# Optimization experiments

Hardware: AMD Instinct MI355X
Metric: run time of the kernel (lower is better)

## Reference

```python
import jax, jax.numpy as jnp
import numpy as np
from jax import lax

IN_CHANNELS = 4
STEPS_IN_ITR = 3


def one_step_ltm(x, T):
    # x: [B, H, W]; T: [B, 10, H, W] (9 stencil weight planes + bias plane)
    B, H, W = x.shape
    xp = jnp.pad(x, ((0, 0), (1, 1), (1, 1)))
    out = T[:, 9]
    k = 0
    # original ordering: X0..X2 scan row-offset with col-offset 0, X3..X5 col 1, X6..X8 col 2
    for dj in range(3):
        for di in range(3):
            out = out + xp[:, di:di + H, dj:dj + W] * T[:, k]
            k += 1
    return out


def setup_inputs() -> dict:
    key = jax.random.key(0)
    k1, k2, k3 = jax.random.split(key, 3)
    B, Tt, C, H, W = 8, 16, 1, 512, 512
    x = jax.random.uniform(k1, (B, Tt, C, H, W), dtype=jnp.float32)
    # stand-in unet: 3x3 SAME conv, in_channels -> 10
    W_unet = jax.random.normal(k2, (10, IN_CHANNELS, 3, 3), dtype=jnp.float32) * 0.1
    b_unet = jax.random.normal(k3, (10,), dtype=jnp.float32) * 0.1
    return {"x": x, "W_unet": W_unet, "b_unet": b_unet}


def reference(x, W_unet, b_unet):
    B, Tt, C, H, W = x.shape
    x_in = x[:, -IN_CHANNELS:, 0]  # [B, in_channels, H, W]
    T = lax.conv_general_dilated(
        x_in, W_unet, window_strides=(1, 1), padding='SAME',
        dimension_numbers=('NCHW', 'OIHW', 'NCHW')) + b_unet[None, :, None, None]

    xt0 = one_step_ltm(x[:, -1, 0], T)  # stored at t=0 WITHOUT sigmoid (as in original)

    def body(xt, _):
        for _j in range(STEPS_IN_ITR):
            xt = one_step_ltm(xt, T)
            xt = jax.nn.sigmoid(one_step_ltm(xt, T))
        return xt, xt

    _, xs = lax.scan(body, xt0, None, length=Tt - 1)  # [Tt-1, B, H, W]
    seq = jnp.concatenate([xt0[None], xs], axis=0)     # [Tt, B, H, W]
    seq = jnp.transpose(seq, (1, 0, 2, 3))             # [B, Tt, H, W]
    xout = jnp.zeros((B, Tt, C, H, W), dtype=x.dtype).at[:, :, 0].set(seq)
    return xout
```

## Files before the change

### kernel.cpp

```cpp
#include <hip/hip_runtime.h>
#include <hip/hip_fp16.h>
#include <math.h>

#define Bd 8
#define Td 16
#define Hd 512
#define Wd 512
#define HWc (Hd * Wd)
#define NPIX (Bd * HWc)

#define CTW 128
#define CTH 8
#define CRW 130
#define CRH 10
#define CPITCH 132
#define CTHR 512

#define TS   64
#define H6   6
#define RS   76
#define LP   77
#define NTHR 768
#define RPG  8
#define NG   10

__global__ __launch_bounds__(CTHR)
void conv_step0_kernel(const float* __restrict__ x,
                       const float* __restrict__ Wu,
                       const float* __restrict__ bu,
                       __half2* __restrict__ T,
                       float* __restrict__ out) {
    __shared__ __align__(16) float sX[4][CRH][CPITCH];

    int bx  = blockIdx.x;
    int b   = bx >> 8;
    int rem = bx & 255;
    int by  = rem >> 2;
    int bc  = rem & 3;
    int i0  = by * CTH;
    int j0  = bc * CTW;

    const float* xb = x + ((size_t)b * Td + 12) * HWc;
    int tid = threadIdx.x;

    for (int idx = tid; idx < 4 * CRH * CRW; idx += CTHR) {
        int ch = idx / (CRH * CRW);
        int r2 = idx - ch * (CRH * CRW);
        int r  = r2 / CRW;
        int c  = r2 - r * CRW;
        int gi = i0 + r - 1, gj = j0 + c - 1;
        float v = 0.0f;
        if ((unsigned)gi < (unsigned)Hd && (unsigned)gj < (unsigned)Wd)
            v = xb[(size_t)ch * HWc + gi * Wd + gj];
        sX[ch][r][c] = v;
    }
    __syncthreads();

    int tx = tid & 63;
    int ty = tid >> 6;

    float t0[10], t1[10];
    #pragma unroll
    for (int o = 0; o < 10; ++o) { float bv = bu[o]; t0[o] = bv; t1[o] = bv; }

    #pragma unroll
    for (int ch = 0; ch < 4; ++ch)
        #pragma unroll
        for (int kh = 0; kh < 3; ++kh) {
            const float* rp = &sX[ch][ty + kh][2 * tx];
            float2 a  = *(const float2*)rp;
            float2 b2 = *(const float2*)(rp + 2);
            float w0 = a.x, w1 = a.y, w2 = b2.x, w3 = b2.y;
            #pragma unroll
            for (int o = 0; o < 10; ++o) {
                float wt0 = Wu[((o * 4 + ch) * 3 + kh) * 3 + 0];
                float wt1 = Wu[((o * 4 + ch) * 3 + kh) * 3 + 1];
                float wt2 = Wu[((o * 4 + ch) * 3 + kh) * 3 + 2];
                t0[o] += w0 * wt0 + w1 * wt1 + w2 * wt2;
                t1[o] += w1 * wt0 + w2 * wt1 + w3 * wt2;
            }
        }

    int gi = i0 + ty;
    int gjv = j0 + 2 * tx;
    size_t pix = (size_t)gi * Wd + gjv;
    __half2* Tb = T + (size_t)b * 5 * HWc;
    #pragma unroll
    for (int q = 0; q < 5; ++q) {
        __half2 h0 = __floats2half2_rn(t0[2 * q], t0[2 * q + 1]);
        __half2 h1 = __floats2half2_rn(t1[2 * q], t1[2 * q + 1]);
        uint2 pk;
        pk.x = *(unsigned*)&h0;
        pk.y = *(unsigned*)&h1;
        *(uint2*)(Tb + (size_t)q * HWc + pix) = pk;
    }

    float o0 = t0[9], o1 = t1[9];
    #pragma unroll
    for (int di = 0; di < 3; ++di) {
        const float* rp = &sX[3][ty + di][2 * tx];
        float2 a  = *(const float2*)rp;
        float2 b2 = *(const float2*)(rp + 2);
        float w0 = a.x, w1 = a.y, w2 = b2.x, w3 = b2.y;
        #pragma unroll
        for (int dj = 0; dj < 3; ++dj) {
            float xa = (dj == 0) ? w0 : ((dj == 1) ? w1 : w2);
            float xc = (dj == 0) ? w1 : ((dj == 1) ? w2 : w3);
            o0 += xa * t0[dj * 3 + di];
            o1 += xc * t1[dj * 3 + di];
        }
    }
    float2 ov; ov.x = o0; ov.y = o1;
    *(float2*)(out + (size_t)b * Td * HWc + pix) = ov;
}

__global__ __launch_bounds__(NTHR, 6)
void fused6_vstrip_kernel(const float* __restrict__ xin,
                          const __half2* __restrict__ T,
                          float* __restrict__ xout) {
    __shared__ float sA[RS * LP];
    __shared__ float sB[RS * LP];

    int tile = blockIdx.x;
    int b   = tile >> 6;
    int trr = (tile >> 3) & 7;
    int tcc = tile & 7;
    int ri = trr * TS - H6;
    int rj = tcc * TS - H6;

    const float* xb = xin + (size_t)b * Td * HWc;
    const __half2* Tb = T + (size_t)b * 5 * HWc;
    int tid = threadIdx.x;

    for (int idx = tid; idx < RS * RS; idx += NTHR) {
        int r = idx / RS, c = idx - r * RS;
        int gi = ri + r, gj = rj + c;
        float v = 0.0f;
        if ((unsigned)gi < (unsigned)Hd && (unsigned)gj < (unsigned)Wd)
            v = xb[gi * Wd + gj];
        sA[r * LP + c] = v;
    }
    for (int idx = tid; idx < 4 * RS; idx += NTHR) {
        int side = idx / RS, k = idx - side * RS;
        int r, c;
        if (side == 0)      { r = 0;      c = k; }
        else if (side == 1) { r = RS - 1; c = k; }
        else if (side == 2) { r = k;      c = 0; }
        else                { r = k;      c = RS - 1; }
        sB[r * LP + c] = 0.0f;
    }

    int g  = tid / RS;
    int c  = tid - g * RS;
    int rs = 1 + g * RPG;
    bool colint = (c >= 1) && (c <= RS - 2);
    bool active = (g < NG) && colint;
    int  gj     = rj + c;
    bool colin  = (unsigned)gj < (unsigned)Wd;

    __half2 treg[RPG][5];
    #pragma unroll
    for (int jj = 0; jj < RPG; ++jj) {
        int r  = rs + jj;
        int gi = ri + r;
        bool ok = active && (r <= RS - 2) && ((unsigned)gi < (unsigned)Hd) && colin;
        #pragma unroll
        for (int q = 0; q < 5; ++q)
            treg[jj][q] = ok ? Tb[(size_t)q * HWc + gi * Wd + gj]
                             : __floats2half2_rn(0.0f, 0.0f);
    }
    __syncthreads();

    float* cur = sA;
    float* nxt = sB;

    #pragma unroll
    for (int s = 1; s <= 6; ++s) {
        if (active) {
            float w00 = cur[(rs - 1) * LP + c - 1];
            float w01 = cur[(rs - 1) * LP + c];
            float w02 = cur[(rs - 1) * LP + c + 1];
            float w10 = cur[rs * LP + c - 1];
            float w11 = cur[rs * LP + c];
            float w12 = cur[rs * LP + c + 1];
            #pragma unroll
            for (int jj = 0; jj < RPG; ++jj) {
                int r  = rs + jj;
                int r2 = (r + 1 <= RS - 1) ? (r + 1) : (RS - 1);
                float w20 = cur[r2 * LP + c - 1];
                float w21 = cur[r2 * LP + c];
                float w22 = cur[r2 * LP + c + 1];

                float2 p0 = __half22float2(treg[jj][0]);
                float2 p1 = __half22float2(treg[jj][1]);
                float2 p2 = __half22float2(treg[jj][2]);
                float2 p3 = __half22float2(treg[jj][3]);
                float2 p4 = __half22float2(treg[jj][4]);

                float a = p4.y
                        + w00 * p0.x + w10 * p0.y + w20 * p1.x
                        + w01 * p1.y + w11 * p2.x + w21 * p2.y
                        + w02 * p3.x + w12 * p3.y + w22 * p4.x;
                if ((s & 1) == 0) a = 1.0f / (1.0f + __expf(-a));

                int gi = ri + r;
                bool rowok = (r <= RS - 2);
                bool inimg = ((unsigned)gi < (unsigned)Hd) && colin;
                if (rowok) nxt[r * LP + c] = inimg ? a : 0.0f;

                w00 = w10; w01 = w11; w02 = w12;
                w10 = w20; w11 = w21; w12 = w22;
            }
        }
        __syncthreads();
        float* tmp = cur; cur = nxt; nxt = tmp;
    }

    float* ob = xout + (size_t)b * Td * HWc;
    for (int idx = tid; idx < TS * TS; idx += NTHR) {
        int rr = idx >> 6, cc = idx & 63;
        ob[(ri + H6 + rr) * Wd + (rj + H6 + cc)] = cur[(H6 + rr) * LP + (H6 + cc)];
    }
}

extern "C" void kernel_launch(void* const* d_in, const int* in_sizes, int n_in,
                              void* d_out, int out_size, void* d_ws, size_t ws_size,
                              hipStream_t stream) {
    const float* x  = (const float*)d_in[0];
    const float* Wu = (const float*)d_in[1];
    const float* bu = (const float*)d_in[2];
    float* out = (float*)d_out;
    __half2* T = (__half2*)d_ws;

    conv_step0_kernel<<<2048, CTHR, 0, stream>>>(x, Wu, bu, T, out);

    for (int t = 1; t < Td; ++t)
        fused6_vstrip_kernel<<<512, NTHR, 0, stream>>>(out + (size_t)(t - 1) * HWc, T,
                                                       out + (size_t)t * HWc);
}
```

Measured before the change: 572.6 us.

## Replace per-timestep launches with persistent cooperative kernel using grid sync

Replaces the 15 separate per-timestep stencil kernel launches with one cooperative persistent kernel of 256 blocks, each handling two tiles and looping over timesteps with grid.sync between them. The T coefficients for both tiles are loaded into registers once and kept across all timesteps, removing repeated T reads and launch gaps. In exchange, register pressure roughly doubles for treg, occupancy drops, and each grid-wide barrier adds synchronization cost. The two tiles per block are processed serially.

```diff
diff --git a/kernel.cpp b/kernel.cpp
--- a/kernel.cpp
+++ b/kernel.cpp
@@ -1,6 +1,9 @@
 #include <hip/hip_runtime.h>
 #include <hip/hip_fp16.h>
+#include <hip/hip_cooperative_groups.h>
 #include <math.h>
+
+namespace cg = cooperative_groups;
 
 #define Bd 8
 #define Td 16
@@ -112,6 +115,134 @@
     }
     float2 ov; ov.x = o0; ov.y = o1;
     *(float2*)(out + (size_t)b * Td * HWc + pix) = ov;
+}
+
+__global__ __launch_bounds__(NTHR, 4)
+void scan_persistent2_kernel(const __half2* __restrict__ T,
+                             float* __restrict__ out) {
+    cg::grid_group grid = cg::this_grid();
+
+    __shared__ float sA[RS * LP];
+    __shared__ float sB[RS * LP];
+
+    int tid = threadIdx.x;
+
+    for (int idx = tid; idx < 4 * RS; idx += NTHR) {
+        int side = idx / RS, k = idx - side * RS;
+        int r, c;
+        if (side == 0)      { r = 0;      c = k; }
+        else if (side == 1) { r = RS - 1; c = k; }
+        else if (side == 2) { r = k;      c = 0; }
+        else                { r = k;      c = RS - 1; }
+        sB[r * LP + c] = 0.0f;
+    }
+
+    int g  = tid / RS;
+    int c  = tid - g * RS;
+    int rs = 1 + g * RPG;
+    bool colint = (c >= 1) && (c <= RS - 2);
+    bool active = (g < NG) && colint;
+
+    int  ri_[2], rj_[2], b_[2];
+    bool colin_[2];
+    __half2 treg[2][RPG][5];
+    #pragma unroll
+    for (int tt = 0; tt < 2; ++tt) {
+        int tile = blockIdx.x + tt * 256;
+        int b   = tile >> 6;
+        int trr = (tile >> 3) & 7;
+        int tcc = tile & 7;
+        b_[tt]  = b;
+        ri_[tt] = trr * TS - H6;
+        rj_[tt] = tcc * TS - H6;
+        int gj  = rj_[tt] + c;
+        colin_[tt] = (unsigned)gj < (unsigned)Wd;
+        const __half2* Tb = T + (size_t)b * 5 * HWc;
+        #pragma unroll
+        for (int jj = 0; jj < RPG; ++jj) {
+            int r  = rs + jj;
+            int gi = ri_[tt] + r;
+            bool ok = active && (r <= RS - 2) &&
+                      ((unsigned)gi < (unsigned)Hd) && colin_[tt];
+            #pragma unroll
+            for (int q = 0; q < 5; ++q)
+                treg[tt][jj][q] = ok ? Tb[(size_t)q * HWc + gi * Wd + gj]
+                                     : __floats2half2_rn(0.0f, 0.0f);
+        }
+    }
+
+    for (int t = 1; t < Td; ++t) {
+        #pragma unroll
+        for (int tt = 0; tt < 2; ++tt) {
+            int ri = ri_[tt], rj = rj_[tt];
+            bool colin = colin_[tt];
+
+            const float* xb = out + ((size_t)b_[tt] * Td + (t - 1)) * HWc;
+            for (int idx = tid; idx < RS * RS; idx += NTHR) {
+                int r = idx / RS, cc = idx - r * RS;
+                int gi2 = ri + r, gj2 = rj + cc;
+                float v = 0.0f;
+                if ((unsigned)gi2 < (unsigned)Hd && (unsigned)gj2 < (unsigned)Wd)
+                    v = xb[gi2 * Wd + gj2];
+                sA[r * LP + cc] = v;
+            }
+            __syncthreads();
+
+            float* cur = sA;
+            float* nxt = sB;
+
+            #pragma unroll
+            for (int s = 1; s <= 6; ++s) {
+                if (active) {
+                    float w00 = cur[(rs - 1) * LP + c - 1];
+                    float w01 = cur[(rs - 1) * LP + c];
+                    float w02 = cur[(rs - 1) * LP + c + 1];
+                    float w10 = cur[rs * LP + c - 1];
+                    float w11 = cur[rs * LP + c];
+                    float w12 = cur[rs * LP + c + 1];
+                    #pragma unroll
+                    for (int jj = 0; jj < RPG; ++jj) {
+                        int r  = rs + jj;
+                        int r2 = (r + 1 <= RS - 1) ? (r + 1) : (RS - 1);
+                        float w20 = cur[r2 * LP + c - 1];
+                        float w21 = cur[r2 * LP + c];
+                        float w22 = cur[r2 * LP + c + 1];
+
+                        float2 p0 = __half22float2(treg[tt][jj][0]);
+                        float2 p1 = __half22float2(treg[tt][jj][1]);
+                        float2 p2 = __half22float2(treg[tt][jj][2]);
+                        float2 p3 = __half22float2(treg[tt][jj][3]);
+                        float2 p4 = __half22float2(treg[tt][jj][4]);
+
+                        float a = p4.y
+                                + w00 * p0.x + w10 * p0.y + w20 * p1.x
+                                + w01 * p1.y + w11 * p2.x + w21 * p2.y
+                                + w02 * p3.x + w12 * p3.y + w22 * p4.x;
+                        if ((s & 1) == 0) a = 1.0f / (1.0f + __expf(-a));
+
+                        int gi2 = ri + r;
+                        bool rowok = (r <= RS - 2);
+                        bool inimg = ((unsigned)gi2 < (unsigned)Hd) && colin;
+                        if (rowok) nxt[r * LP + c] = inimg ? a : 0.0f;
+
+                        w00 = w10; w01 = w11; w02 = w12;
+                        w10 = w20; w11 = w21; w12 = w22;
+                    }
+                }
+                __syncthreads();
+                float* tmp = cur; cur = nxt; nxt = tmp;
+            }
+
+            float* ob = out + ((size_t)b_[tt] * Td + t) * HWc;
+            for (int idx = tid; idx < TS * TS; idx += NTHR) {
+                int rr = idx >> 6, cc = idx & 63;
+                ob[(ri + H6 + rr) * Wd + (rj + H6 + cc)] =
+                    sA[(H6 + rr) * LP + (H6 + cc)];
+            }
+            __syncthreads();
+        }
+        grid.sync();
+    }
 }
 
 __global__ __launch_bounds__(NTHR, 6)
@@ -234,6 +365,21 @@
 
     conv_step0_kernel<<<2048, CTHR, 0, stream>>>(x, Wu, bu, T, out);
 
+    int nb = 0;
+    hipError_t qe = hipOccupancyMaxActiveBlocksPerMultiprocessor(
+        &nb, scan_persistent2_kernel, NTHR, 0);
+    bool coop_ok = (qe == hipSuccess) && (nb >= 1);
+
+    if (coop_ok) {
+        const __half2* Tc = T;
+        float* oc = out;
+        void* args[] = { (void*)&Tc, (void*)&oc };
+        hipError_t le = hipLaunchCooperativeKernel(
+            (const void*)scan_persistent2_kernel,
+            dim3(256), dim3(NTHR), args, 0, stream);
+        if (le == hipSuccess) return;
+    }
+
     for (int t = 1; t < Td; ++t)
         fused6_vstrip_kernel<<<512, NTHR, 0, stream>>>(out + (size_t)(t - 1) * HWc, T,
                                                        out + (size_t)t * HWc);
```

After: 573.0 us. No clear change (+0.1%).

## Use taller 128x64 tiles with single in-place shared buffer and 1024 threads

Applied to the files above, without the earlier changes.

Replaces the 64x64 tile stencil kernel with a 128x64-core tile (140x76 with halo), launched as 256 blocks of 1024 threads, each thread handling 11 rows. The ping-pong shared buffers become one buffer updated in place: results are held in registers and written after an extra barrier. The T prefetch is now issued before the input tile load so the two overlap. This cuts halo recompute and shared memory per block, but halves the block count to 256, below the GPU's CU count, and adds a second barrier per step.

```diff
diff --git a/kernel.cpp b/kernel.cpp
--- a/kernel.cpp
+++ b/kernel.cpp
@@ -16,13 +16,15 @@
 #define CPITCH 132
 #define CTHR 512
 
-#define TS   64
-#define H6   6
-#define RS   76
-#define LP   77
-#define NTHR 768
-#define RPG  8
-#define NG   10
+#define FCR 128
+#define FCC 64
+#define FH  6
+#define FTR 140
+#define FTC 76
+#define FLP 77
+#define FTHR 1024
+#define FRPG 11
+#define FNG 13
 
 __global__ __launch_bounds__(CTHR)
 void conv_step0_kernel(const float* __restrict__ x,
@@ -114,82 +116,70 @@
     *(float2*)(out + (size_t)b * Td * HWc + pix) = ov;
 }
 
-__global__ __launch_bounds__(NTHR, 6)
-void fused6_vstrip_kernel(const float* __restrict__ xin,
-                          const __half2* __restrict__ T,
-                          float* __restrict__ xout) {
-    __shared__ float sA[RS * LP];
-    __shared__ float sB[RS * LP];
+__global__ __launch_bounds__(FTHR)
+void fused6_bigtile_kernel(const float* __restrict__ xin,
+                           const __half2* __restrict__ T,
+                           float* __restrict__ xout) {
+    __shared__ float sA[FTR * FLP];
 
     int tile = blockIdx.x;
-    int b   = tile >> 6;
-    int trr = (tile >> 3) & 7;
-    int tcc = tile & 7;
-    int ri = trr * TS - H6;
-    int rj = tcc * TS - H6;
+    int b  = tile >> 5;
+    int tr = (tile >> 3) & 3;
+    int tc = tile & 7;
+    int ri = tr * FCR - FH;
+    int rj = tc * FCC - FH;
 
     const float* xb = xin + (size_t)b * Td * HWc;
     const __half2* Tb = T + (size_t)b * 5 * HWc;
     int tid = threadIdx.x;
 
-    for (int idx = tid; idx < RS * RS; idx += NTHR) {
-        int r = idx / RS, c = idx - r * RS;
-        int gi = ri + r, gj = rj + c;
-        float v = 0.0f;
-        if ((unsigned)gi < (unsigned)Hd && (unsigned)gj < (unsigned)Wd)
-            v = xb[gi * Wd + gj];
-        sA[r * LP + c] = v;
-    }
-    for (int idx = tid; idx < 4 * RS; idx += NTHR) {
-        int side = idx / RS, k = idx - side * RS;
-        int r, c;
-        if (side == 0)      { r = 0;      c = k; }
-        else if (side == 1) { r = RS - 1; c = k; }
-        else if (side == 2) { r = k;      c = 0; }
-        else                { r = k;      c = RS - 1; }
-        sB[r * LP + c] = 0.0f;
-    }
-
-    int g  = tid / RS;
-    int c  = tid - g * RS;
-    int rs = 1 + g * RPG;
-    bool colint = (c >= 1) && (c <= RS - 2);
-    bool active = (g < NG) && colint;
+    int g  = tid / FTC;
+    int c  = tid - g * FTC;
+    int rs = 1 + g * FRPG;
+    bool active = (g < FNG) && (c >= 1) && (c <= FTC - 2);
     int  gj     = rj + c;
     bool colin  = (unsigned)gj < (unsigned)Wd;
 
-    __half2 treg[RPG][5];
-    #pragma unroll
-    for (int jj = 0; jj < RPG; ++jj) {
+    __half2 treg[FRPG][5];
+    #pragma unroll
+    for (int jj = 0; jj < FRPG; ++jj) {
         int r  = rs + jj;
         int gi = ri + r;
-        bool ok = active && (r <= RS - 2) && ((unsigned)gi < (unsigned)Hd) && colin;
+        bool ok = active && (r <= FTR - 2) &&
+                  ((unsigned)gi < (unsigned)Hd) && colin;
         #pragma unroll
         for (int q = 0; q < 5; ++q)
             treg[jj][q] = ok ? Tb[(size_t)q * HWc + gi * Wd + gj]
                              : __floats2half2_rn(0.0f, 0.0f);
     }
+
+    for (int idx = tid; idx < FTR * FTC; idx += FTHR) {
+        int r = idx / FTC, cc = idx - r * FTC;
+        int gi2 = ri + r, gj2 = rj + cc;
+        float v = 0.0f;
+        if ((unsigned)gi2 < (unsigned)Hd && (unsigned)gj2 < (unsigned)Wd)
+            v = xb[gi2 * Wd + gj2];
+        sA[r * FLP + cc] = v;
+    }
     __syncthreads();
 
-    float* cur = sA;
-    float* nxt = sB;
-
     #pragma unroll
     for (int s = 1; s <= 6; ++s) {
+        float nv[FRPG];
         if (active) {
-            float w00 = cur[(rs - 1) * LP + c - 1];
-            float w01 = cur[(rs - 1) * LP + c];
-            float w02 = cur[(rs - 1) * LP + c + 1];
-            float w10 = cur[rs * LP + c - 1];
-            float w11 = cur[rs * LP + c];
-            float w12 = cur[rs * LP + c + 1];
+            float w00 = sA[(rs - 1) * FLP + c - 1];
+            float w01 = sA[(rs - 1) * FLP + c];
+            float w02 = sA[(rs - 1) * FLP + c + 1];
+            float w10 = sA[rs * FLP + c - 1];
+            float w11 = sA[rs * FLP + c];
+            float w12 = sA[rs * FLP + c + 1];
             #pragma unroll
-            for (int jj = 0; jj < RPG; ++jj) {
+            for (int jj = 0; jj < FRPG; ++jj) {
                 int r  = rs + jj;
-                int r2 = (r + 1 <= RS - 1) ? (r + 1) : (RS - 1);
-                float w20 = cur[r2 * LP + c - 1];
-                float w21 = cur[r2 * LP + c];
-                float w22 = cur[r2 * LP + c + 1];
+                int r2 = (r + 1 <= FTR - 1) ? (r + 1) : (FTR - 1);
+                float w20 = sA[r2 * FLP + c - 1];
+                float w21 = sA[r2 * FLP + c];
+                float w22 = sA[r2 * FLP + c + 1];
 
                 float2 p0 = __half22float2(treg[jj][0]);
                 float2 p1 = __half22float2(treg[jj][1]);
@@ -203,23 +193,30 @@
                         + w02 * p3.x + w12 * p3.y + w22 * p4.x;
                 if ((s & 1) == 0) a = 1.0f / (1.0f + __expf(-a));
 
-                int gi = ri + r;
-                bool rowok = (r <= RS - 2);
-                bool inimg = ((unsigned)gi < (unsigned)Hd) && colin;
-                if (rowok) nxt[r * LP + c] = inimg ? a : 0.0f;
+                int gi2 = ri + r;
+                bool inimg = ((unsigned)gi2 < (unsigned)Hd) && colin;
+                nv[jj] = inimg ? a : 0.0f;
 
                 w00 = w10; w01 = w11; w02 = w12;
                 w10 = w20; w11 = w21; w12 = w22;
             }
         }
         __syncthreads();
-        float* tmp = cur; cur = nxt; nxt = tmp;
+        if (active) {
+            #pragma unroll
+            for (int jj = 0; jj < FRPG; ++jj) {
+                int r = rs + jj;
+                if (r <= FTR - 2) sA[r * FLP + c] = nv[jj];
+            }
+        }
+        __syncthreads();
     }
 
     float* ob = xout + (size_t)b * Td * HWc;
-    for (int idx = tid; idx < TS * TS; idx += NTHR) {
+    for (int idx = tid; idx < FCR * FCC; idx += FTHR) {
         int rr = idx >> 6, cc = idx & 63;
-        ob[(ri + H6 + rr) * Wd + (rj + H6 + cc)] = cur[(H6 + rr) * LP + (H6 + cc)];
+        ob[(ri + FH + rr) * Wd + (rj + FH + cc)] =
+            sA[(FH + rr) * FLP + (FH + cc)];
     }
 }
 
@@ -235,6 +232,6 @@
     conv_step0_kernel<<<2048, CTHR, 0, stream>>>(x, Wu, bu, T, out);
 
     for (int t = 1; t < Td; ++t)
-        fused6_vstrip_kernel<<<512, NTHR, 0, stream>>>(out + (size_t)(t - 1) * HWc, T,
-                                                       out + (size_t)t * HWc);
+        fused6_bigtile_kernel<<<256, FTHR, 0, stream>>>(out + (size_t)(t - 1) * HWc, T,
+                                                        out + (size_t)t * HWc);
 }
```

Measured after the change: 1.076 ms. +87.9%, slower.

## Enlarge stencil tiles to 128x64 and compute 2x2 outputs per conv thread

Applied to the files above, without the earlier changes.

The fused six-step stencil kernel now uses 128x64 output tiles with 1024 threads and 11 rows per thread group. This cuts the redundant halo recomputation per output, since the 6-row halo is amortised over a taller tile. The conv kernel computes a 2x2 pixel block per thread and reuses the loaded 4x4 window across rows. The trade-offs are fewer blocks (256 per step, 1024 for conv), lower occupancy, and higher register pressure from the larger treg array.

```diff
diff --git a/kernel.cpp b/kernel.cpp
--- a/kernel.cpp
+++ b/kernel.cpp
@@ -9,45 +9,47 @@
 #define HWc (Hd * Wd)
 #define NPIX (Bd * HWc)
 
-#define CTW 128
-#define CTH 8
-#define CRW 130
-#define CRH 10
-#define CPITCH 132
-#define CTHR 512
-
-#define TS   64
-#define H6   6
-#define RS   76
-#define LP   77
-#define NTHR 768
-#define RPG  8
-#define NG   10
-
-__global__ __launch_bounds__(CTHR)
+#define VTW 128
+#define VTH 16
+#define VRW 130
+#define VRH 18
+#define VP  132
+#define VTHR 512
+
+#define WCR 128
+#define WCC 64
+#define WH  6
+#define WTR 140
+#define WTC 76
+#define WLP 77
+#define WTHR 1024
+#define WRPG 11
+#define WNG 13
+
+__global__ __launch_bounds__(VTHR, 4)
 void conv_step0_kernel(const float* __restrict__ x,
                        const float* __restrict__ Wu,
                        const float* __restrict__ bu,
                        __half2* __restrict__ T,
                        float* __restrict__ out) {
-    __shared__ __align__(16) float sX[4][CRH][CPITCH];
+    __shared__ __align__(16) float sX[4][VRH][VP];
 
     int bx  = blockIdx.x;
-    int b   = bx >> 8;
-    int rem = bx & 255;
+    int b   = bx >> 7;
+    int rem = bx & 127;
     int by  = rem >> 2;
     int bc  = rem & 3;
-    int i0  = by * CTH;
-    int j0  = bc * CTW;
+    int i0  = by * VTH;
+    int j0  = bc * VTW;
 
     const float* xb = x + ((size_t)b * Td + 12) * HWc;
     int tid = threadIdx.x;
 
-    for (int idx = tid; idx < 4 * CRH * CRW; idx += CTHR) {
-        int ch = idx / (CRH * CRW);
-        int r2 = idx - ch * (CRH * CRW);
-        int r  = r2 / CRW;
-        int c  = r2 - r * CRW;
+    for (int idx = tid; idx < 4 * VRH * VRW; idx += VTHR) {
+        int ch = idx / (VRH * VRW);
+        int r2 = idx - ch * (VRH * VRW);
+        int r  = r2 / VRW;
+        int c  = r2 - r * VRW;
         int gi = i0 + r - 1, gj = j0 + c - 1;
         float v = 0.0f;
         if ((unsigned)gi < (unsigned)Hd && (unsigned)gj < (unsigned)Wd)
@@ -59,111 +61,125 @@
     int tx = tid & 63;
     int ty = tid >> 6;
 
-    float t0[10], t1[10];
-    #pragma unroll
-    for (int o = 0; o < 10; ++o) { float bv = bu[o]; t0[o] = bv; t1[o] = bv; }
-
-    #pragma unroll
-    for (int ch = 0; ch < 4; ++ch)
-        #pragma unroll
-        for (int kh = 0; kh < 3; ++kh) {
-            const float* rp = &sX[ch][ty + kh][2 * tx];
+    float t00[10], t01[10], t10[10], t11[10];
+    #pragma unroll
+    for (int o = 0; o < 10; ++o) {
+        float bv = bu[o];
+        t00[o] = bv; t01[o] = bv; t10[o] = bv; t11[o] = bv;
+    }
+
+    float w[4][4];
+    #pragma unroll
+    for (int ch = 0; ch < 4; ++ch) {
+        #pragma unroll
+        for (int rr = 0; rr < 4; ++rr) {
+            const float* rp = &sX[ch][2 * ty + rr][2 * tx];
             float2 a  = *(const float2*)rp;
             float2 b2 = *(const float2*)(rp + 2);
-            float w0 = a.x, w1 = a.y, w2 = b2.x, w3 = b2.y;
+            w[rr][0] = a.x; w[rr][1] = a.y; w[rr][2] = b2.x; w[rr][3] = b2.y;
+        }
+        #pragma unroll
+        for (int kh = 0; kh < 3; ++kh) {
             #pragma unroll
             for (int o = 0; o < 10; ++o) {
                 float wt0 = Wu[((o * 4 + ch) * 3 + kh) * 3 + 0];
                 float wt1 = Wu[((o * 4 + ch) * 3 + kh) * 3 + 1];
                 float wt2 = Wu[((o * 4 + ch) * 3 + kh) * 3 + 2];
-                t0[o] += w0 * wt0 + w1 * wt1 + w2 * wt2;
-                t1[o] += w1 * wt0 + w2 * wt1 + w3 * wt2;
+                t00[o] += w[kh][0] * wt0 + w[kh][1] * wt1 + w[kh][2] * wt2;
+                t01[o] += w[kh][1] * wt0 + w[kh][2] * wt1 + w[kh][3] * wt2;
+                t10[o] += w[kh + 1][0] * wt0 + w[kh + 1][1] * wt1 + w[kh + 1][2] * wt2;
+                t11[o] += w[kh + 1][1] * wt0 + w[kh + 1][2] * wt1 + w[kh + 1][3] * wt2;
             }
         }
-
-    int gi = i0 + ty;
-    int gjv = j0 + 2 * tx;
-    size_t pix = (size_t)gi * Wd + gjv;
+    }
+
+    int gi0 = i0 + 2 * ty;
+    int gj0 = j0 + 2 * tx;
+    size_t pix0 = (size_t)gi0 * Wd + gj0;
+    size_t pix1 = pix0 + Wd;
     __half2* Tb = T + (size_t)b * 5 * HWc;
     #pragma unroll
     for (int q = 0; q < 5; ++q) {
-        __half2 h0 = __floats2half2_rn(t0[2 * q], t0[2 * q + 1]);
-        __half2 h1 = __floats2half2_rn(t1[2 * q], t1[2 * q + 1]);
-        uint2 pk;
-        pk.x = *(unsigned*)&h0;
-        pk.y = *(unsigned*)&h1;
-        *(uint2*)(Tb + (size_t)q * HWc + pix) = pk;
-    }
-
-    float o0 = t0[9], o1 = t1[9];
-    #pragma unroll
-    for (int di = 0; di < 3; ++di) {
-        const float* rp = &sX[3][ty + di][2 * tx];
-        float2 a  = *(const float2*)rp;
-        float2 b2 = *(const float2*)(rp + 2);
-        float w0 = a.x, w1 = a.y, w2 = b2.x, w3 = b2.y;
-        #pragma unroll
-        for (int dj = 0; dj < 3; ++dj) {
-            float xa = (dj == 0) ? w0 : ((dj == 1) ? w1 : w2);
-            float xc = (dj == 0) ? w1 : ((dj == 1) ? w2 : w3);
-            o0 += xa * t0[dj * 3 + di];
-            o1 += xc * t1[dj * 3 + di];
-        }
-    }
-    float2 ov; ov.x = o0; ov.y = o1;
-    *(float2*)(out + (size_t)b * Td * HWc + pix) = ov;
+        __half2 a0 = __floats2half2_rn(t00[2 * q], t00[2 * q + 1]);
+        __half2 a1 = __floats2half2_rn(t01[2 * q], t01[2 * q + 1]);
+        __half2 b0 = __floats2half2_rn(t10[2 * q], t10[2 * q + 1]);
+        __half2 b1 = __floats2half2_rn(t11[2 * q], t11[2 * q + 1]);
+        uint2 p0, p1;
+        p0.x = *(unsigned*)&a0; p0.y = *(unsigned*)&a1;
+        p1.x = *(unsigned*)&b0; p1.y = *(unsigned*)&b1;
+        *(uint2*)(Tb + (size_t)q * HWc + pix0) = p0;
+        *(uint2*)(Tb + (size_t)q * HWc + pix1) = p1;
+    }
+
+    float o00 = t00[9], o01 = t01[9], o10 = t10[9], o11 = t11[9];
+    #pragma unroll
+    for (int dj = 0; dj < 3; ++dj)
+        #pragma unroll
+        for (int di = 0; di < 3; ++di) {
+            int k = dj * 3 + di;
+            o00 += w[di][dj]         * t00[k];
+            o01 += w[di][dj + 1]     * t01[k];
+            o10 += w[di + 1][dj]     * t10[k];
+            o11 += w[di + 1][dj + 1] * t11[k];
+        }
+    float* ob = out + (size_t)b * Td * HWc;
+    float2 v0; v0.x = o00; v0.y = o01;
+    float2 v1; v1.x = o10; v1.y = o11;
+    *(float2*)(ob + pix0) = v0;
+    *(float2*)(ob + pix1) = v1;
 }
 
-__global__ __launch_bounds__(NTHR, 6)
-void fused6_vstrip_kernel(const float* __restrict__ xin,
-                          const __half2* __restrict__ T,
-                          float* __restrict__ xout) {
-    __shared__ float sA[RS * LP];
-    __shared__ float sB[RS * LP];
+__global__ __launch_bounds__(WTHR, 4)
+void fused6_wide_kernel(const float* __restrict__ xin,
+                        const __half2* __restrict__ T,
+                        float* __restrict__ xout) {
+    __shared__ float sA[WTR * WLP];
+    __shared__ float sB[WTR * WLP];
 
     int tile = blockIdx.x;
-    int b   = tile >> 6;
-    int trr = (tile >> 3) & 7;
-    int tcc = tile & 7;
-    int ri = trr * TS - H6;
-    int rj = tcc * TS - H6;
+    int b  = tile >> 5;
+    int tr = (tile >> 3) & 3;
+    int tc = tile & 7;
+    int ri = tr * WCR - WH;
+    int rj = tc * WCC - WH;
 
     const float* xb = xin + (size_t)b * Td * HWc;
     const __half2* Tb = T + (size_t)b * 5 * HWc;
     int tid = threadIdx.x;
 
-    for (int idx = tid; idx < RS * RS; idx += NTHR) {
-        int r = idx / RS, c = idx - r * RS;
+    for (int idx = tid; idx < WTR * WTC; idx += WTHR) {
+        int r = idx / WTC, c = idx - r * WTC;
         int gi = ri + r, gj = rj + c;
         float v = 0.0f;
         if ((unsigned)gi < (unsigned)Hd && (unsigned)gj < (unsigned)Wd)
             v = xb[gi * Wd + gj];
-        sA[r * LP + c] = v;
-    }
-    for (int idx = tid; idx < 4 * RS; idx += NTHR) {
-        int side = idx / RS, k = idx - side * RS;
-        int r, c;
-        if (side == 0)      { r = 0;      c = k; }
-        else if (side == 1) { r = RS - 1; c = k; }
-        else if (side == 2) { r = k;      c = 0; }
-        else                { r = k;      c = RS - 1; }
-        sB[r * LP + c] = 0.0f;
-    }
-
-    int g  = tid / RS;
-    int c  = tid - g * RS;
-    int rs = 1 + g * RPG;
-    bool colint = (c >= 1) && (c <= RS - 2);
-    bool active = (g < NG) && colint;
+        sA[r * WLP + c] = v;
+    }
+    for (int idx = tid; idx < 2 * WTC; idx += WTHR) {
+        int r = (idx < WTC) ? 0 : (WTR - 1);
+        int c = (idx < WTC) ? idx : idx - WTC;
+        sB[r * WLP + c] = 0.0f;
+    }
+    for (int idx = tid; idx < 2 * WTR; idx += WTHR) {
+        int r = (idx < WTR) ? idx : idx - WTR;
+        int c = (idx < WTR) ? 0 : (WTC - 1);
+        sB[r * WLP + c] = 0.0f;
+    }
+
+    int g  = tid / WTC;
+    int c  = tid - g * WTC;
+    int rs = 1 + g * WRPG;
+    bool colint = (c >= 1) && (c <= WTC - 2);
+    bool active = (g < WNG) && colint;
     int  gj     = rj + c;
     bool colin  = (unsigned)gj < (unsigned)Wd;
 
-    __half2 treg[RPG][5];
-    #pragma unroll
-    for (int jj = 0; jj < RPG; ++jj) {
+    __half2 treg[WRPG][5];
+    #pragma unroll
+    for (int jj = 0; jj < WRPG; ++jj) {
         int r  = rs + jj;
         int gi = ri + r;
-        bool ok = active && (r <= RS - 2) && ((unsigned)gi < (unsigned)Hd) && colin;
+        bool ok = active && (r <= WTR - 2) && ((unsigned)gi < (unsigned)Hd) && colin;
         #pragma unroll
         for (int q = 0; q < 5; ++q)
             treg[jj][q] = ok ? Tb[(size_t)q * HWc + gi * Wd + gj]
@@ -177,19 +193,19 @@
     #pragma unroll
     for (int s = 1; s <= 6; ++s) {
         if (active) {
-            float w00 = cur[(rs - 1) * LP + c - 1];
-            float w01 = cur[(rs - 1) * LP + c];
-            float w02 = cur[(rs - 1) * LP + c + 1];
-            float w10 = cur[rs * LP + c - 1];
-            float w11 = cur[rs * LP + c];
-            float w12 = cur[rs * LP + c + 1];
+            float w00 = cur[(rs - 1) * WLP + c - 1];
+            float w01 = cur[(rs - 1) * WLP + c];
+            float w02 = cur[(rs - 1) * WLP + c + 1];
+            float w10 = cur[rs * WLP + c - 1];
+            float w11 = cur[rs * WLP + c];
+            float w12 = cur[rs * WLP + c + 1];
             #pragma unroll
-            for (int jj = 0; jj < RPG; ++jj) {
+            for (int jj = 0; jj < WRPG; ++jj) {
                 int r  = rs + jj;
-                int r2 = (r + 1 <= RS - 1) ? (r + 1) : (RS - 1);
-                float w20 = cur[r2 * LP + c - 1];
-                float w21 = cur[r2 * LP + c];
-                float w22 = cur[r2 * LP + c + 1];
+                int r2 = (r + 1 <= WTR - 1) ? (r + 1) : (WTR - 1);
+                float w20 = cur[r2 * WLP + c - 1];
+                float w21 = cur[r2 * WLP + c];
+                float w22 = cur[r2 * WLP + c + 1];
 
                 float2 p0 = __half22float2(treg[jj][0]);
                 float2 p1 = __half22float2(treg[jj][1]);
@@ -204,9 +220,9 @@
                 if ((s & 1) == 0) a = 1.0f / (1.0f + __expf(-a));
 
                 int gi = ri + r;
-                bool rowok = (r <= RS - 2);
+                bool rowok = (r <= WTR - 2);
                 bool inimg = ((unsigned)gi < (unsigned)Hd) && colin;
-                if (rowok) nxt[r * LP + c] = inimg ? a : 0.0f;
+                if (rowok) nxt[r * WLP + c] = inimg ? a : 0.0f;
 
                 w00 = w10; w01 = w11; w02 = w12;
                 w10 = w20; w11 = w21; w12 = w22;
@@ -217,9 +233,9 @@
     }
 
     float* ob = xout + (size_t)b * Td * HWc;
-    for (int idx = tid; idx < TS * TS; idx += NTHR) {
+    for (int idx = tid; idx < WCR * WCC; idx += WTHR) {
         int rr = idx >> 6, cc = idx & 63;
-        ob[(ri + H6 + rr) * Wd + (rj + H6 + cc)] = cur[(H6 + rr) * LP + (H6 + cc)];
+        ob[(ri + WH + rr) * Wd + (rj + WH + cc)] = cur[(WH + rr) * WLP + (WH + cc)];
     }
 }
 
@@ -232,9 +248,9 @@
     float* out = (float*)d_out;
     __half2* T = (__half2*)d_ws;
 
-    conv_step0_kernel<<<2048, CTHR, 0, stream>>>(x, Wu, bu, T, out);
+    conv_step0_kernel<<<1024, VTHR, 0, stream>>>(x, Wu, bu, T, out);
 
     for (int t = 1; t < Td; ++t)
-        fused6_vstrip_kernel<<<512, NTHR, 0, stream>>>(out + (size_t)(t - 1) * HWc, T,
-                                                       out + (size_t)t * HWc);
+        fused6_wide_kernel<<<256, WTHR, 0, stream>>>(out + (size_t)(t - 1) * HWc, T,
+                                                     out + (size_t)t * HWc);
 }
```

Result: faster. 546.7 us (-4.5%).
